# Optimization experiments

Measured on AMD Instinct MI355X. Metric: run time of the kernel, lower is better.

## Reference

```python
import jax, jax.numpy as jnp
import numpy as np

# ---- model dims ----
D_MODEL = 256; D_STATE = 128; D_CONV = 4; EXPAND = 2; HEADDIM = 64
D_INNER = EXPAND * D_MODEL            # 512
NHEADS = D_INNER // HEADDIM           # 8
CONV_DIM = D_INNER + 2 * D_STATE      # 768
D_IN_PROJ = 2 * D_INNER + 2 * D_STATE + NHEADS  # 1288
N_GENES = 4095; BATCH = 4; CHUNK = 64
GENE_ID_DIM = 64; PATH_DIM = 128; CHR_DIM = 16; N_CHROM = 25; LFF = 32
GENE_FEAT_DIM = GENE_ID_DIM + PATH_DIM + 2 * CHR_DIM  # 224
N_PERT = 2048; PERT_DIM = 128


def silu(x):
    return x * jax.nn.sigmoid(x)


def segsum_exp(a):
    # a: (..., T). Returns lower-triangular exp(sum_{k=j+1..i} a_k), zero above diag.
    T = a.shape[-1]
    cs = jnp.cumsum(a, axis=-1)
    d = cs[..., :, None] - cs[..., None, :]
    mask = jnp.tril(jnp.ones((T, T), dtype=bool))
    return jnp.exp(jnp.where(mask, d, 0.0)) * mask


def ssd(X, A, B, C):
    # Chunked SSD (Mamba2 selective scan). X:(b,l,h,p) pre-multiplied by dt,
    # A:(b,l,h) = a*dt, B/C:(b,l,n) (ngroups=1 broadcast over heads).
    b, l, h, p = X.shape
    n = B.shape[-1]
    c = l // CHUNK
    Xc = X.reshape(b, c, CHUNK, h, p)
    Bc = B.reshape(b, c, CHUNK, n)
    Cc = C.reshape(b, c, CHUNK, n)
    Ac = A.reshape(b, c, CHUNK, h).transpose(0, 3, 1, 2)  # (b,h,c,cl)
    A_cs = jnp.cumsum(Ac, axis=-1)
    L = segsum_exp(Ac)                                     # (b,h,c,cl,cl)
    Y_diag = jnp.einsum('bcln,bcsn,bhcls,bcshp->bclhp', Cc, Bc, L, Xc)
    decay_states = jnp.exp(A_cs[..., -1:] - A_cs)          # (b,h,c,cl)
    states = jnp.einsum('bcln,bhcl,bclhp->bchpn', Bc, decay_states, Xc)
    chunk_decay = jnp.exp(A_cs[..., -1])                   # (b,h,c)

    def step(h_prev, inp):
        dec, s = inp
        return h_prev * dec[..., None, None] + s, h_prev

    init = jnp.zeros((b, h, p, n), X.dtype)
    _, prev = jax.lax.scan(step, init, (chunk_decay.transpose(2, 0, 1),
                                        states.transpose(1, 0, 2, 3, 4)))
    prev = prev.transpose(1, 0, 2, 3, 4)                   # (b,c,h,p,n)
    Y_off = jnp.einsum('bcln,bchpn,bhcl->bclhp', Cc, prev, jnp.exp(A_cs))
    return (Y_diag + Y_off).reshape(b, l, h, p)


def mamba2(x, in_w, conv_w, conv_b, dt_bias, A_log, D, norm_w, out_w):
    b, l, _ = x.shape
    zxbcdt = x @ in_w.T                                    # (b,l,1288)
    z = zxbcdt[..., :D_INNER]
    xBC = zxbcdt[..., D_INNER:D_INNER + CONV_DIM]
    dt = jax.nn.softplus(zxbcdt[..., D_INNER + CONV_DIM:] + dt_bias)  # (b,l,h)
    # causal depthwise conv1d
    xc = jax.lax.conv_general_dilated(
        xBC.transpose(0, 2, 1), conv_w[:, None, :], (1,), [(D_CONV - 1, 0)],
        feature_group_count=CONV_DIM,
        dimension_numbers=('NCH', 'OIH', 'NCH'))
    xBC = silu(xc.transpose(0, 2, 1) + conv_b)
    xs = xBC[..., :D_INNER].reshape(b, l, NHEADS, HEADDIM)
    Bm = xBC[..., D_INNER:D_INNER + D_STATE]
    Cm = xBC[..., D_INNER + D_STATE:]
    A = -jnp.exp(A_log)                                    # (h,)
    y = ssd(xs * dt[..., None], dt * A, Bm, Cm) + D[:, None] * xs
    y = y.reshape(b, l, D_INNER)
    y = y * silu(z)                                        # gated RMSNorm
    y = y * jax.lax.rsqrt(jnp.mean(y * y, axis=-1, keepdims=True) + 1e-5) * norm_w
    return y @ out_w.T


def _forward(perturbation_idx, chr_idx, locus_fourier, pathway_features,
             gene_id_emb, chr_emb, locus_w, locus_b, pert_emb, cond_w, cond_b,
             inp_w, inp_b, ln_g, ln_b,
             mf_in_w, mf_conv_w, mf_conv_b, mf_dt_bias, mf_A_log, mf_D, mf_norm_w, mf_out_w,
             mb_in_w, mb_conv_w, mb_conv_b, mb_dt_bias, mb_A_log, mb_D, mb_norm_w, mb_out_w,
             head_w, head_b):
    e_locus = jax.nn.gelu(locus_fourier @ locus_w.T + locus_b, approximate=False)
    gene_feat = jnp.concatenate(
        [gene_id_emb, pathway_features, chr_emb[chr_idx], e_locus], axis=-1)  # (G,224)
    cond = pert_emb[perturbation_idx] @ cond_w.T + cond_b                      # (B,224)
    seq = jnp.concatenate(
        [cond[:, None, :],
         jnp.broadcast_to(gene_feat[None], (BATCH, N_GENES, GENE_FEAT_DIM))], axis=1)
    seq = seq @ inp_w.T + inp_b                                                # (B,4096,256)
    mu = jnp.mean(seq, axis=-1, keepdims=True)
    var = jnp.var(seq, axis=-1, keepdims=True)
    seq = (seq - mu) * jax.lax.rsqrt(var + 1e-5) * ln_g + ln_b
    # L = 4096 is already a multiple of 16 -> no padding branch.
    h_fwd = mamba2(seq, mf_in_w, mf_conv_w, mf_conv_b, mf_dt_bias, mf_A_log, mf_D, mf_norm_w, mf_out_w)
    h_bwd = jnp.flip(mamba2(jnp.flip(seq, 1), mb_in_w, mb_conv_w, mb_conv_b, mb_dt_bias, mb_A_log, mb_D, mb_norm_w, mb_out_w), 1)
    H = h_fwd + h_bwd
    return H[:, 1:, :] @ head_w.T + head_b                                     # (B,4095,1)


def setup_inputs() -> dict:
    key = jax.random.key(0)
    ks = iter(jax.random.split(key, 64))

    def nrm(shape, s=0.02):
        return jax.random.normal(next(ks), shape, jnp.float32) * s

    inp = {}
    inp['perturbation_idx'] = jax.random.randint(next(ks), (BATCH,), 0, N_PERT)
    inp['chr_idx'] = jax.random.randint(next(ks), (N_GENES,), 0, N_CHROM)
    inp['locus_fourier'] = nrm((N_GENES, 2 * LFF), 1.0)
    inp['pathway_features'] = nrm((N_GENES, PATH_DIM), 1.0)
    inp['gene_id_emb'] = nrm((N_GENES, GENE_ID_DIM))
    inp['chr_emb'] = nrm((N_CHROM, CHR_DIM))
    inp['locus_w'] = nrm((CHR_DIM, 2 * LFF)); inp['locus_b'] = jnp.zeros((CHR_DIM,))
    inp['pert_emb'] = nrm((N_PERT, PERT_DIM))
    inp['cond_w'] = nrm((GENE_FEAT_DIM, PERT_DIM)); inp['cond_b'] = jnp.zeros((GENE_FEAT_DIM,))
    inp['inp_w'] = nrm((D_MODEL, GENE_FEAT_DIM)); inp['inp_b'] = jnp.zeros((D_MODEL,))
    inp['ln_g'] = jnp.ones((D_MODEL,)); inp['ln_b'] = jnp.zeros((D_MODEL,))
    for pre in ('mf_', 'mb_'):
        inp[pre + 'in_w'] = nrm((D_IN_PROJ, D_MODEL))
        inp[pre + 'conv_w'] = nrm((CONV_DIM, D_CONV), 0.2)
        inp[pre + 'conv_b'] = jnp.zeros((CONV_DIM,))
        inp[pre + 'dt_bias'] = nrm((NHEADS,), 0.5)
        inp[pre + 'A_log'] = jnp.log(jax.random.uniform(next(ks), (NHEADS,), jnp.float32, 1.0, 16.0))
        inp[pre + 'D'] = jnp.ones((NHEADS,))
        inp[pre + 'norm_w'] = jnp.ones((D_INNER,))
        inp[pre + 'out_w'] = nrm((D_MODEL, D_INNER))
    inp['head_w'] = nrm((1, D_MODEL)); inp['head_b'] = jnp.zeros((1,))
    return inp


def reference(perturbation_idx, chr_idx, locus_fourier, pathway_features,
              gene_id_emb, chr_emb, locus_w, locus_b, pert_emb, cond_w, cond_b,
              inp_w, inp_b, ln_g, ln_b,
              mf_in_w, mf_conv_w, mf_conv_b, mf_dt_bias, mf_A_log, mf_D, mf_norm_w, mf_out_w,
              mb_in_w, mb_conv_w, mb_conv_b, mb_dt_bias, mb_A_log, mb_D, mb_norm_w, mb_out_w,
              head_w, head_b):
    return _forward(perturbation_idx, chr_idx, locus_fourier, pathway_features,
                    gene_id_emb, chr_emb, locus_w, locus_b, pert_emb, cond_w, cond_b,
                    inp_w, inp_b, ln_g, ln_b,
                    mf_in_w, mf_conv_w, mf_conv_b, mf_dt_bias, mf_A_log, mf_D, mf_norm_w, mf_out_w,
                    mb_in_w, mb_conv_w, mb_conv_b, mb_dt_bias, mb_A_log, mb_D, mb_norm_w, mb_out_w,
                    head_w, head_b)
```

## Files before the change

### kernel.cpp

```cpp
#include <hip/hip_runtime.h>
#include <hip/hip_bf16.h>
#include <math.h>

#define LSEQ   4096
#define NGENES 4095
#define NB     4
#define DM     256
#define DI     512
#define DST    128
#define NH     8
#define HD     64
#define CONVD  768
#define DIP    1288
#define NCHK   64
#define CHK    64
#define GFD    224

#define ZN  ((size_t)NB*LSEQ*DI)
#define XN  ((size_t)NB*LSEQ*CONVD)
#define DN  ((size_t)NB*LSEQ*NH)
#define AN  ((size_t)NB*NH*LSEQ)
#define SN  ((size_t)NB*NCHK*NH*HD*DST)
#define GN  ((size_t)NB*NCHK*CHK*CHK)
#define BTN ((size_t)NB*NCHK*DST*CHK)
#define HN  ((size_t)NB*LSEQ*DM)

typedef short bf16x8 __attribute__((ext_vector_type(8)));
typedef short bf16x4 __attribute__((ext_vector_type(4)));
typedef float f32x4 __attribute__((ext_vector_type(4)));

__device__ __forceinline__ float bf2f(unsigned short u){
    unsigned int x = ((unsigned int)u) << 16;
    return __uint_as_float(x);
}
__device__ __forceinline__ unsigned short f2bf(float f){
    __hip_bfloat16 h = __float2bfloat16(f);
    return *reinterpret_cast<unsigned short*>(&h);
}

typedef const __attribute__((address_space(1))) void* gas_t;
typedef __attribute__((address_space(3))) void* las_t;
__device__ __forceinline__ void gload16(const void* g, void* l){
    __builtin_amdgcn_global_load_lds((gas_t)g, (las_t)l, 16, 0, 0);
}

__global__ void k_detect(const unsigned int* p, int* flag){
    *flag = (*p == 0x3F803F80u) ? 1 : 0;
}

struct ConvAll { const void* src[31]; float* dst[31]; int n[31]; };
__global__ void k_convert_all(ConvAll a, const int* flag){
    int ai = blockIdx.y;
    int n = a.n[ai];
    const void* s = a.src[ai]; float* d = a.dst[ai];
    bool bf = (*flag != 0);
    for(int i = blockIdx.x*256 + threadIdx.x; i < n; i += gridDim.x*256){
        d[i] = bf ? bf2f(((const unsigned short*)s)[i]) : ((const float*)s)[i];
    }
}

struct PackAll { const void* src[4]; unsigned short* dst[4]; int n[4]; };
__global__ void k_pack_all(PackAll a, const int* flag){
    int ai = blockIdx.y;
    int n = a.n[ai];
    const void* s = a.src[ai]; unsigned short* d = a.dst[ai];
    bool bf = (*flag != 0);
    for(int i = blockIdx.x*256 + threadIdx.x; i < n; i += gridDim.x*256){
        if(bf) d[i] = ((const unsigned short*)s)[i];
        else   d[i] = f2bf(((const float*)s)[i]);
    }
}

__global__ void k_packw256(const void* src, unsigned short* dst, const int* flag){
    int row = blockIdx.x, col = threadIdx.x;
    unsigned short v = 0;
    if(col < GFD){
        if(*flag) v = ((const unsigned short*)src)[row*GFD + col];
        else      v = f2bf(((const float*)src)[row*GFD + col]);
    }
    dst[row*256 + col] = v;
}

__global__ void k_genefeat(const float* gene_id, const float* pathway, const float* chr_emb,
                           const int* chr_idx, const float* lf, const float* locus_w,
                           const float* locus_b, unsigned short* gfb){
    int g = blockIdx.x; int t = threadIdx.x;
    float v = 0.f;
    if(t < 64)       v = gene_id[g*64 + t];
    else if(t < 192) v = pathway[g*128 + (t-64)];
    else if(t < 208) v = chr_emb[chr_idx[g]*16 + (t-192)];
    else if(t < 224){
        int j = t - 208;
        float acc = locus_b[j];
        for(int k=0;k<64;k++) acc += lf[g*64+k]*locus_w[j*64+k];
        v = 0.5f*acc*(1.0f + erff(acc*0.7071067811865475f));
    }
    gfb[g*256 + t] = f2bf(v);
}

__global__ void k_cond(const int* pidx, const float* pert_emb, const float* cond_w,
                       const float* cond_b, unsigned short* condb){
    int b = blockIdx.x, t = threadIdx.x;
    float acc = 0.f;
    if(t < GFD){
        const float* pe = pert_emb + pidx[b]*128;
        acc = cond_b[t];
        for(int k=0;k<128;k++) acc += pe[k]*cond_w[t*128+k];
    }
    condb[b*256 + t] = f2bf(acc);
}

__global__ __launch_bounds__(256) void k_mm_seqpre(const unsigned short* gfb,
            const unsigned short* condb, const unsigned short* Wb,
            const float* inp_b, float* seq_pre){
    __shared__ unsigned short sh[16384];
    int sblk = (blockIdx.x & 7)*32 + (blockIdx.x >> 3);
    int bm = sblk>>1, bn = sblk&1;
    int m0 = bm*128, n0 = bn*128;
    int t = threadIdx.x, lane = t&63;
    int wid = t>>6, wm = wid>>1, wn = wid&1;
    int fr = lane&15, fk = lane>>4;
    int srow = t>>3;
    int scol = ((t&7) ^ (srow&7))*8;
    const unsigned short* gA[4]; const unsigned short* gB[4];
#pragma unroll
    for(int q=0;q<4;q++){
        int row = q*32 + srow;
        int m = m0+row; int b = m>>12, l = m&4095;
        gA[q] = l ? &gfb[(size_t)(l-1)*256 + scol] : &condb[(size_t)b*256 + scol];
        gB[q] = &Wb[(size_t)(n0+row)*256 + scol];
    }
    unsigned short* lA = &sh[t*8];
    unsigned short* lB = &sh[8192 + t*8];
    f32x4 acc[4][4];
#pragma unroll
    for(int i=0;i<4;i++)
#pragma unroll
        for(int j=0;j<4;j++) acc[i][j] = (f32x4){0.f,0.f,0.f,0.f};
    for(int it=0; it<4; it++){
#pragma unroll
        for(int q=0;q<4;q++){
            gload16(gA[q], lA + q*2048);
            gload16(gB[q], lB + q*2048);
            gA[q] += 64; gB[q] += 64;
        }
        __syncthreads();
#pragma unroll
        for(int kk8=0;kk8<8;kk8+=4){
            bf16x8 av[4], bv[4];
#pragma unroll
            for(int i=0;i<4;i++){
                int r = wm*64+i*16+fr;
                av[i] = *(bf16x8*)&sh[r*64 + (((kk8+fk)^(r&7))*8)];
            }
#pragma unroll
            for(int j=0;j<4;j++){
                int r = wn*64+j*16+fr;
                bv[j] = *(bf16x8*)&sh[8192 + r*64 + (((kk8+fk)^(r&7))*8)];
            }
#pragma unroll
            for(int i=0;i<4;i++)
#pragma unroll
                for(int j=0;j<4;j++)
                    acc[i][j] = __builtin_amdgcn_mfma_f32_16x16x32_bf16(av[i], bv[j], acc[i][j], 0,0,0);
        }
        __syncthreads();
    }
#pragma unroll
    for(int i=0;i<4;i++)
#pragma unroll
        for(int rr=0;rr<4;rr++){
            int m = m0 + wm*64 + i*16 + fk*4 + rr;
#pragma unroll
            for(int j=0;j<4;j++){
                int n = n0 + wn*64 + j*16 + fr;
                seq_pre[(size_t)m*256 + n] = acc[i][j][rr] + inp_b[n];
            }
        }
}

__global__ void k_ln(const float* seq_pre, const float* ln_g, const float* ln_b,
                     unsigned short* seqb){
    int t = threadIdx.x; int w = t>>6, lane = t&63;
    int m = blockIdx.x*4 + w;
    f32x4 v = *(const f32x4*)&seq_pre[(size_t)m*256 + lane*4];
    float s1 = v[0]+v[1]+v[2]+v[3];
    float s2 = v[0]*v[0]+v[1]*v[1]+v[2]*v[2]+v[3]*v[3];
#pragma unroll
    for(int o=32;o>0;o>>=1){ s1 += __shfl_xor(s1,o,64); s2 += __shfl_xor(s2,o,64); }
    float mu  = s1*(1.f/256.f);
    float var = s2*(1.f/256.f) - mu*mu;
    float rs = rsqrtf(var+1e-5f);
    unsigned short o4[4];
#pragma unroll
    for(int j=0;j<4;j++){
        int n = lane*4+j;
        o4[j] = f2bf((v[j]-mu)*rs*ln_g[n] + ln_b[n]);
    }
    *(unsigned long long*)&seqb[(size_t)m*256 + lane*4] = *(unsigned long long*)o4;
}

__global__ __launch_bounds__(256) void k_mm_inproj(const unsigned short* seqb,
            const unsigned short* W0, const unsigned short* W1,
            const float* dtb0, const float* dtb1,
            unsigned short* zbase, unsigned short* xbase, float* dtbase){
    __shared__ unsigned short sh[16384];
    int blk = (blockIdx.x & 7)*352 + (blockIdx.x >> 3);
    int dir = blk >= 1408; int inner = blk - dir*1408;
    int bm = inner/11, bn = inner%11;
    int m0 = bm*128, n0 = bn*128;
    const unsigned short* Wb = dir ? W1 : W0;
    const float* dt_bias = dir ? dtb1 : dtb0;
    unsigned short* zb   = zbase + (size_t)dir*ZN;
    unsigned short* xbcr = xbase + (size_t)dir*XN;
    float* dtb = dtbase + (size_t)dir*DN;
    int t = threadIdx.x, lane = t&63;
    int wid = t>>6, wm = wid>>1, wn = wid&1;
    int fr = lane&15, fk = lane>>4;
    int srow = t>>3;
    int scol = ((t&7) ^ (srow&7))*8;
    const unsigned short* gA[4]; const unsigned short* gB[4];
#pragma unroll
    for(int q=0;q<4;q++){
        int row = q*32 + srow;
        int m = m0+row; int b = m>>12, l = m&4095;
        int ml = dir ? (4095-l) : l;
        gA[q] = &seqb[(size_t)(b*4096+ml)*256 + scol];
        gB[q] = &Wb[(size_t)(n0+row)*256 + scol];
    }
    unsigned short* lA = &sh[t*8];
    unsigned short* lB = &sh[8192 + t*8];
    f32x4 acc[4][4];
#pragma unroll
    for(int i=0;i<4;i++)
#pragma unroll
        for(int j=0;j<4;j++) acc[i][j] = (f32x4){0.f,0.f,0.f,0.f};
    for(int it=0; it<4; it++){
#pragma unroll
        for(int q=0;q<4;q++){
            gload16(gA[q], lA + q*2048);
            gload16(gB[q], lB + q*2048);
            gA[q] += 64; gB[q] += 64;
        }
        __syncthreads();
#pragma unroll
        for(int kk8=0;kk8<8;kk8+=4){
            bf16x8 av[4], bv[4];
#pragma unroll
            for(int i=0;i<4;i++){
                int r = wm*64+i*16+fr;
                av[i] = *(bf16x8*)&sh[r*64 + (((kk8+fk)^(r&7))*8)];
            }
#pragma unroll
            for(int j=0;j<4;j++){
                int r = wn*64+j*16+fr;
                bv[j] = *(bf16x8*)&sh[8192 + r*64 + (((kk8+fk)^(r&7))*8)];
            }
#pragma unroll
            for(int i=0;i<4;i++)
#pragma unroll
                for(int j=0;j<4;j++)
                    acc[i][j] = __builtin_amdgcn_mfma_f32_16x16x32_bf16(av[i], bv[j], acc[i][j], 0,0,0);
        }
        __syncthreads();
    }
    if(bn == 10){
#pragma unroll
        for(int i=0;i<4;i++)
#pragma unroll
            for(int rr=0;rr<4;rr++){
                int m = m0 + wm*64 + i*16 + fk*4 + rr;
#pragma unroll
                for(int j=0;j<4;j++){
                    int n = n0 + wn*64 + j*16 + fr;
                    if(n >= DIP) continue;
                    int hh = n - 1280;
                    float x = acc[i][j][rr] + dt_bias[hh];
                    dtb[(size_t)m*NH + hh] = (x > 20.f) ? x : log1pf(expf(x));
                }
            }
        return;
    }
    unsigned short* dst; int stride, coff;
    if(bn < 4){ dst = zb;   stride = DI;    coff = bn*128; }
    else      { dst = xbcr; stride = CONVD; coff = bn*128 - 512; }
#pragma unroll
    for(int p=0;p<2;p++){
        if(wm == p){
#pragma unroll
            for(int i=0;i<4;i++)
#pragma unroll
                for(int j=0;j<4;j++)
#pragma unroll
                    for(int rr=0;rr<4;rr++){
                        int row = i*16 + fk*4 + rr;
                        int col = wn*64 + j*16 + fr;
                        sh[row*136 + col] = f2bf(acc[i][j][rr]);
                    }
        }
        __syncthreads();
#pragma unroll
        for(int k=0;k<4;k++){
            int idx = t + k*256;
            int row = idx>>4, c8 = (idx&15)*8;
            bf16x8 v = *(bf16x8*)&sh[row*136 + c8];
            *(bf16x8*)&dst[(size_t)(m0+p*64+row)*stride + coff + c8] = v;
        }
        __syncthreads();
    }
}

__global__ __launch_bounds__(256) void k_conv(const unsigned short* xbase,
        const float* cw0, const float* cw1, const float* cb0, const float* cb1,
        unsigned short* obase){
    __shared__ unsigned short raw[19*768];
    __shared__ float cwf[4*768];
    __shared__ float cbf[768];
    int blk = blockIdx.x;
    int dir = blk>>10; int rem = blk&1023;
    int b = rem>>8, rg = rem&255;
    const unsigned short* xr = xbase + (size_t)dir*XN;
    unsigned short* out = obase + (size_t)dir*XN;
    const float* cw = dir ? cw1 : cw0;
    const float* cb = dir ? cb1 : cb0;
    int l0 = rg*16;
    int t = threadIdx.x;
    for(int i=t;i<3072;i+=256){ int q=i/768, c=i%768; cwf[q*768+c] = cw[c*4+q]; }
    for(int i=t;i<768;i+=256) cbf[i] = cb[i];
    for(int i=t;i<19*96;i+=256){
        int r = i/96, c8 = (i%96)*8;
        int l = l0 - 3 + r;
        bf16x8 v = (bf16x8){0,0,0,0,0,0,0,0};
        if(l >= 0) v = *(const bf16x8*)&xr[(size_t)(b*4096+l)*768 + c8];
        *(bf16x8*)&raw[r*768 + c8] = v;
    }
    __syncthreads();
    for(int i=t;i<16*96;i+=256){
        int r = i/96, c8 = (i%96)*8;
        bf16x8 o;
#pragma unroll
        for(int j=0;j<8;j++){
            int c = c8+j;
            float acc = cbf[c];
#pragma unroll
            for(int q=0;q<4;q++) acc += cwf[q*768+c]*bf2f(raw[(r+q)*768 + c]);
            o[j] = (short)f2bf(acc/(1.f+__expf(-acc)));
        }
        *(bf16x8*)&out[(size_t)(b*4096+l0+r)*768 + c8] = o;
    }
}

__global__ void k_cumsum(const float* dtbase, const float* Al0, const float* Al1,
                         float* acsbase){
    __shared__ float tmp[64];
    int blk = blockIdx.x;
    int dir = blk>>11; int rem = blk&2047;
    int c = rem & 63; int bh = rem >> 6; int h = bh & 7; int b = bh >> 3;
    const float* dtb = dtbase + (size_t)dir*DN;
    float* acs = acsbase + (size_t)dir*AN;
    int s = threadIdx.x;
    float A = -expf((dir?Al1:Al0)[h]);
    int l = c*64 + s;
    tmp[s] = dtb[(size_t)(b*4096+l)*NH + h] * A;
    __syncthreads();
    if(s == 0){ for(int i=1;i<64;i++) tmp[i] += tmp[i-1]; }
    __syncthreads();
    acs[(size_t)(b*8+h)*4096 + l] = tmp[s];
}

__global__ __launch_bounds__(256) void k_cbprep(const unsigned short* xbase,
        unsigned short* Gbase, unsigned short* BTbase){
    __shared__ unsigned short Bb[64][136];
    __shared__ unsigned short Cb[64][136];
    __shared__ unsigned short BTs[128][72];
    int blk = blockIdx.x;
    int dir = blk>>8; int bc = blk&255;
    int b = bc>>6, c = bc&63;
    const unsigned short* xbcb = xbase + (size_t)dir*XN;
    unsigned short* Gb = Gbase + (size_t)dir*GN;
    unsigned short* BTg = BTbase + (size_t)dir*BTN;
    int t = threadIdx.x, lane = t&63, wid = t>>6;
    int fr = lane&15, fk = lane>>4;
    size_t rowbase = (size_t)(b*4096 + c*64)*CONVD;
#pragma unroll
    for(int q=0;q<4;q++){
        int e = t + q*256; int r = e>>4, ch = (e&15)*8;
        *(bf16x8*)&Bb[r][ch] = *(const bf16x8*)&xbcb[rowbase + (size_t)r*CONVD + 512 + ch];
        *(bf16x8*)&Cb[r][ch] = *(const bf16x8*)&xbcb[rowbase + (size_t)r*CONVD + 640 + ch];
    }
    __syncthreads();
    f32x4 g[4];
#pragma unroll
    for(int j=0;j<4;j++) g[j] = (f32x4){0.f,0.f,0.f,0.f};
#pragma unroll
    for(int k0=0;k0<128;k0+=32){
        bf16x8 av = *(bf16x8*)&Cb[wid*16+fr][k0+fk*8];
#pragma unroll
        for(int j=0;j<4;j++){
            bf16x8 bv = *(bf16x8*)&Bb[j*16+fr][k0+fk*8];
            g[j] = __builtin_amdgcn_mfma_f32_16x16x32_bf16(av, bv, g[j], 0,0,0);
        }
    }
    size_t gbase = (size_t)bc*4096;
#pragma unroll
    for(int j=0;j<4;j++)
#pragma unroll
        for(int rr=0;rr<4;rr++)
            Gb[gbase + (size_t)(wid*16+fk*4+rr)*64 + j*16+fr] = f2bf(g[j][rr]);
#pragma unroll
    for(int q=0;q<4;q++){
        int e = t + q*256; int s = e>>4, n0 = (e&15)*8;
        bf16x8 v = *(bf16x8*)&Bb[s][n0];
#pragma unroll
        for(int j=0;j<8;j++){
            int n = n0 + j;
            BTs[n][s ^ (n&56)] = (unsigned short)v[j];
        }
    }
    __syncthreads();
    size_t btbase = (size_t)bc*8192;
#pragma unroll
    for(int q=0;q<4;q++){
        int e = t + q*256; int n = e>>3, s0 = (e&7)*8;
        bf16x8 v = *(bf16x8*)&BTs[n][s0 ^ (n&56)];
        *(bf16x8*)&BTg[btbase + (size_t)n*64 + s0] = v;
    }
}

#define G_OFF  0
#define BT_OFF 4608
#define XT_OFF 13824
#define MS_OFF 18432
__global__ __launch_bounds__(256) void k_ssd_intra(const unsigned short* xbase,
        const unsigned short* Gbase, const unsigned short* BTbase,
        const float* dtbase, const float* acsbase,
        const float* Dv0, const float* Dv1,
        unsigned short* Ybase, unsigned short* sbase_){
    __shared__ unsigned short sh[23040];
    __shared__ float acs_s[64], dts[64], ws[64];
    int blk = blockIdx.x;
    int dir = blk>>9; int rem = blk&511;
    int hg = rem&1, c = (rem>>1)&63, b = rem>>7;
    int bc = b*64 + c;
    const unsigned short* xbcb = xbase + (size_t)dir*XN;
    const unsigned short* Gb = Gbase + (size_t)dir*GN;
    const unsigned short* BTg = BTbase + (size_t)dir*BTN;
    const float* dtb = dtbase + (size_t)dir*DN;
    const float* acs = acsbase + (size_t)dir*AN;
    const float* Dv = dir ? Dv1 : Dv0;
    unsigned short* Yb = Ybase + (size_t)dir*XN;
    unsigned short* states = sbase_ + (size_t)dir*SN;
    int t = threadIdx.x, lane = t&63, wid = t>>6;
    int wr = wid>>1, wc = wid&1;
    int fr = lane&15, fk = lane>>4;
    size_t rowbase = (size_t)(b*4096 + c*64)*CONVD;
    size_t gbase = (size_t)bc*4096;
    size_t btbase = (size_t)bc*8192;
#pragma unroll
    for(int q=0;q<2;q++){
        int e = t + q*256; int l = e>>3, s0 = (e&7)*8;
        *(bf16x8*)&sh[G_OFF + l*72 + s0] = *(const bf16x8*)&Gb[gbase + (size_t)l*64 + s0];
    }
#pragma unroll
    for(int q=0;q<4;q++){
        int e = t + q*256; int n = e>>3, s0 = (e&7)*8;
        *(bf16x8*)&sh[BT_OFF + n*72 + (s0 ^ (n&56))] = *(const bf16x8*)&BTg[btbase + (size_t)n*64 + s0];
    }
    for(int hh=0; hh<4; hh++){
        int h = hg*4 + hh;
        __syncthreads();
#pragma unroll
        for(int q=0;q<2;q++){
            int e = t + q*256; int s = e>>3, p0 = (e&7)*8;
            bf16x8 v = *(const bf16x8*)&xbcb[rowbase + (size_t)s*CONVD + h*64 + p0];
            int sw = s ^ (p0&56);
#pragma unroll
            for(int j=0;j<8;j++) sh[XT_OFF + (p0+j)*72 + sw] = (unsigned short)v[j];
        }
        if(t < 64){
            acs_s[t] = acs[(size_t)(b*8+h)*4096 + c*64 + t];
            dts[t]   = dtb[(size_t)(b*4096 + c*64 + t)*NH + h];
        }
        __syncthreads();
        if(t < 64) ws[t] = __expf(acs_s[63]-acs_s[t])*dts[t];
#pragma unroll
        for(int q=0;q<16;q++){
            int e = t + q*256; int l = e>>6, s = e&63;
            float m = (s <= l) ? bf2f(sh[G_OFF + l*72 + s])*__expf(acs_s[l]-acs_s[s])*dts[s] : 0.f;
            sh[MS_OFF + l*72 + s] = f2bf(m);
        }
        __syncthreads();
        f32x4 y[2][2];
#pragma unroll
        for(int i=0;i<2;i++)
#pragma unroll
            for(int j=0;j<2;j++) y[i][j] = (f32x4){0.f,0.f,0.f,0.f};
#pragma unroll
        for(int k0=0;k0<64;k0+=32){
            bf16x8 av[2], bv[2];
#pragma unroll
            for(int i=0;i<2;i++) av[i] = *(bf16x8*)&sh[MS_OFF + (wr*32+i*16+fr)*72 + k0+fk*8];
#pragma unroll
            for(int j=0;j<2;j++){
                int p = wc*32+j*16+fr;
                bv[j] = *(bf16x8*)&sh[XT_OFF + p*72 + ((k0+fk*8) ^ (p&56))];
            }
#pragma unroll
            for(int i=0;i<2;i++)
#pragma unroll
                for(int j=0;j<2;j++)
                    y[i][j] = __builtin_amdgcn_mfma_f32_16x16x32_bf16(av[i], bv[j], y[i][j], 0,0,0);
        }
        __syncthreads();
        float Dh = Dv[h];
#pragma unroll
        for(int i=0;i<2;i++)
#pragma unroll
            for(int j=0;j<2;j++)
#pragma unroll
                for(int rr=0;rr<4;rr++){
                    int l = wr*32 + i*16 + fk*4 + rr;
                    int p = wc*32 + j*16 + fr;
                    float xv = bf2f(sh[XT_OFF + p*72 + (l ^ (p&56))]);
                    sh[MS_OFF + l*72 + p] = f2bf(y[i][j][rr] + Dh*xv);
                }
        f32x4 s4[2][4];
#pragma unroll
        for(int i=0;i<2;i++)
#pragma unroll
            for(int j=0;j<4;j++) s4[i][j] = (f32x4){0.f,0.f,0.f,0.f};
#pragma unroll
        for(int k0=0;k0<64;k0+=32){
            bf16x8 av[2], bv[4];
#pragma unroll
            for(int i=0;i<2;i++){
                int p = wr*32+i*16+fr;
                bf16x8 raw = *(bf16x8*)&sh[XT_OFF + p*72 + ((k0+fk*8) ^ (p&56))];
#pragma unroll
                for(int e=0;e<8;e++) av[i][e] = (short)f2bf(bf2f((unsigned short)raw[e]) * ws[k0+fk*8+e]);
            }
#pragma unroll
            for(int j=0;j<4;j++){
                int n = wc*64+j*16+fr;
                bv[j] = *(bf16x8*)&sh[BT_OFF + n*72 + ((k0+fk*8) ^ (n&56))];
            }
#pragma unroll
            for(int i=0;i<2;i++)
#pragma unroll
                for(int j=0;j<4;j++)
                    s4[i][j] = __builtin_amdgcn_mfma_f32_16x16x32_bf16(av[i], bv[j], s4[i][j], 0,0,0);
        }
        __syncthreads();
#pragma unroll
        for(int k=0;k<2;k++){
            int e = t + k*256; int row = e>>3, c8 = (e&7)*8;
            bf16x8 v = *(bf16x8*)&sh[MS_OFF + row*72 + c8];
            *(bf16x8*)&Yb[(size_t)(b*4096 + c*64 + row)*DI + h*64 + c8] = v;
        }
        __syncthreads();
#pragma unroll
        for(int i=0;i<2;i++)
#pragma unroll
            for(int j=0;j<4;j++)
#pragma unroll
                for(int rr=0;rr<4;rr++){
                    int p = wr*32 + i*16 + fk*4 + rr;
                    int n = wc*64 + j*16 + fr;
                    sh[XT_OFF + p*128 + (n ^ ((p&7)<<3))] = f2bf(s4[i][j][rr]);
                }
        __syncthreads();
        size_t sb = ((size_t)bc*8 + h)*8192;
#pragma unroll
        for(int k=0;k<4;k++){
            int e = t + k*256; int p = e>>4, c8 = (e&15)*8;
            bf16x8 v = *(bf16x8*)&sh[XT_OFF + p*128 + (c8 ^ ((p&7)<<3))];
            *(bf16x8*)&states[sb + p*128 + c8] = v;
        }
    }
}

__global__ void k_scan(unsigned short* sbase_, const float* acsbase){
    __shared__ float dec_s[64];
    int blk = blockIdx.x;
    int dir = blk>>8; int rem = blk&255;
    int e8 = rem&7, h = (rem>>3)&7, b = rem>>6;
    unsigned short* states = sbase_ + (size_t)dir*SN;
    const float* acs = acsbase + (size_t)dir*AN;
    int t = threadIdx.x;
    if(t < 64) dec_s[t] = __expf(acs[(size_t)(b*8+h)*4096 + t*64 + 63]);
    __syncthreads();
    int off = e8*1024 + t*4;
    float h4[4] = {0.f,0.f,0.f,0.f};
    size_t base0 = ((size_t)(b*64)*8 + h)*8192 + off;
    for(int c0=0;c0<64;c0+=4){
        bf16x4 v[4];
#pragma unroll
        for(int u=0;u<4;u++)
            v[u] = *(const bf16x4*)&states[base0 + (size_t)(c0+u)*65536];
#pragma unroll
        for(int u=0;u<4;u++){
            float dec = dec_s[c0+u];
            bf16x4 o;
#pragma unroll
            for(int j=0;j<4;j++){
                o[j] = (short)f2bf(h4[j]);
                h4[j] = h4[j]*dec + bf2f((unsigned short)v[u][j]);
            }
            *(bf16x4*)&states[base0 + (size_t)(c0+u)*65536] = o;
        }
    }
}

__global__ __launch_bounds__(256) void k_ssd_off(unsigned short* xbase,
        const unsigned short* sbase_, const float* acsbase){
    __shared__ unsigned short Ct[64][136];
    __shared__ unsigned short Pv[64][136];
    __shared__ float acs_s[64];
    int blk = blockIdx.x;
    int dir = blk>>8; int bc = blk&255;
    int c = bc&63, b = bc>>6;
    unsigned short* xbcb = xbase + (size_t)dir*XN;
    const unsigned short* prev = sbase_ + (size_t)dir*SN;
    const float* acs = acsbase + (size_t)dir*AN;
    int t = threadIdx.x, lane = t&63, wid = t>>6;
    int wr = wid>>1, wc = wid&1;
    int fr = lane&15, fk = lane>>4;
    size_t rowbase = (size_t)(b*4096 + c*64)*CONVD;
    unsigned short* ostg = &Pv[0][0];
#pragma unroll
    for(int q=0;q<4;q++){
        int e = t + q*256;
        int r = e>>4, ch = (e&15)*8;
        *(bf16x8*)&Ct[r][ch] = *(const bf16x8*)&xbcb[rowbase + (size_t)r*CONVD + 640 + ch];
    }
    for(int h=0; h<8; h++){
        size_t sb = ((size_t)bc*8 + h)*8192;
        __syncthreads();
#pragma unroll
        for(int q=0;q<4;q++){
            int e = t + q*256;
            int r = e>>4, ch = (e&15)*8;
            *(bf16x8*)&Pv[r][ch] = *(const bf16x8*)&prev[sb + (size_t)r*128 + ch];
        }
        if(t < 64) acs_s[t] = acs[(size_t)(b*8+h)*4096 + c*64 + t];
        __syncthreads();
        f32x4 o[2][2];
#pragma unroll
        for(int i=0;i<2;i++)
#pragma unroll
            for(int j=0;j<2;j++) o[i][j] = (f32x4){0.f,0.f,0.f,0.f};
        for(int k0=0;k0<128;k0+=32){
            bf16x8 av[2], bv[2];
#pragma unroll
            for(int i=0;i<2;i++) av[i] = *(bf16x8*)&Ct[wr*32+i*16+fr][k0+fk*8];
#pragma unroll
            for(int j=0;j<2;j++) bv[j] = *(bf16x8*)&Pv[wc*32+j*16+fr][k0+fk*8];
#pragma unroll
            for(int i=0;i<2;i++)
#pragma unroll
                for(int j=0;j<2;j++)
                    o[i][j] = __builtin_amdgcn_mfma_f32_16x16x32_bf16(av[i], bv[j], o[i][j], 0,0,0);
        }
        __syncthreads();
#pragma unroll
        for(int i=0;i<2;i++)
#pragma unroll
            for(int j=0;j<2;j++)
#pragma unroll
                for(int rr=0;rr<4;rr++){
                    int l = wr*32 + i*16 + fk*4 + rr;
                    int p = wc*32 + j*16 + fr;
                    ostg[l*72 + p] = f2bf(o[i][j][rr]*__expf(acs_s[l]));
                }
        __syncthreads();
#pragma unroll
        for(int k=0;k<2;k++){
            int e = t + k*256; int row = e>>3, c8 = (e&7)*8;
            bf16x8 v = *(bf16x8*)&ostg[row*72 + c8];
            *(bf16x8*)&xbcb[rowbase + (size_t)row*CONVD + h*64 + c8] = v;
        }
    }
}

__global__ void k_gate(const unsigned short* Ybase, const unsigned short* xbase,
                       const unsigned short* zbase,
                       const float* nw0, const float* nw1, unsigned short* ynbase){
    int blk = blockIdx.x;
    int dir = blk>>12;
    int t = threadIdx.x; int w = t>>6, lane = t&63;
    int m = (blk&4095)*4 + w;
    const unsigned short* Yb = Ybase + (size_t)dir*XN;
    const unsigned short* Ob = xbase + (size_t)dir*XN;
    const unsigned short* zb = zbase + (size_t)dir*ZN;
    unsigned short* ynb = ynbase + (size_t)dir*SN;
    const float* norm_w = dir ? nw1 : nw0;
    size_t base = (size_t)m*DI + lane*8;
    bf16x8 yv = *(const bf16x8*)&Yb[base];
    bf16x8 ov = *(const bf16x8*)&Ob[(size_t)m*CONVD + lane*8];
    bf16x8 zv = *(const bf16x8*)&zb[base];
    float v[8]; float ss = 0.f;
#pragma unroll
    for(int j=0;j<8;j++){
        float zf = bf2f((unsigned short)zv[j]);
        float yt = bf2f((unsigned short)yv[j]) + bf2f((unsigned short)ov[j]);
        float f = yt * (zf/(1.f+__expf(-zf)));
        v[j] = f; ss += f*f;
    }
#pragma unroll
    for(int o=32;o>0;o>>=1) ss += __shfl_xor(ss,o,64);
    float r = rsqrtf(ss*(1.f/512.f) + 1e-5f);
    bf16x8 o8;
#pragma unroll
    for(int j=0;j<8;j++) o8[j] = (short)f2bf(v[j]*r*norm_w[lane*8+j]);
    *(bf16x8*)&ynb[base] = o8;
}

__global__ __launch_bounds__(256) void k_mm_outproj(const unsigned short* ynbase,
            const unsigned short* W0, const unsigned short* W1, float* Hbase){
    __shared__ unsigned short sh[16384];
    int blk = (blockIdx.x & 7)*64 + (blockIdx.x >> 3);
    int dir = blk>>8; int rem = blk&255;
    int bm = rem>>1, bn = rem&1;
    int m0 = bm*128, n0 = bn*128;
    const unsigned short* ynb = ynbase + (size_t)dir*SN;
    const unsigned short* Wb = dir ? W1 : W0;
    float* H = Hbase + (size_t)dir*HN;
    int t = threadIdx.x, lane = t&63;
    int wid = t>>6, wm = wid>>1, wn = wid&1;
    int fr = lane&15, fk = lane>>4;
    int srow = t>>3;
    int scol = ((t&7) ^ (srow&7))*8;
    const unsigned short* gA[4]; const unsigned short* gB[4];
#pragma unroll
    for(int q=0;q<4;q++){
        int row = q*32 + srow;
        gA[q] = &ynb[(size_t)(m0+row)*512 + scol];
        gB[q] = &Wb[(size_t)(n0+row)*512 + scol];
    }
    unsigned short* lA = &sh[t*8];
    unsigned short* lB = &sh[8192 + t*8];
    f32x4 acc[4][4];
#pragma unroll
    for(int i=0;i<4;i++)
#pragma unroll
        for(int j=0;j<4;j++) acc[i][j] = (f32x4){0.f,0.f,0.f,0.f};
    for(int it=0; it<8; it++){
#pragma unroll
        for(int q=0;q<4;q++){
            gload16(gA[q], lA + q*2048);
            gload16(gB[q], lB + q*2048);
            gA[q] += 64; gB[q] += 64;
        }
        __syncthreads();
#pragma unroll
        for(int kk8=0;kk8<8;kk8+=4){
            bf16x8 av[4], bv[4];
#pragma unroll
            for(int i=0;i<4;i++){
                int r = wm*64+i*16+fr;
                av[i] = *(bf16x8*)&sh[r*64 + (((kk8+fk)^(r&7))*8)];
            }
#pragma unroll
            for(int j=0;j<4;j++){
                int r = wn*64+j*16+fr;
                bv[j] = *(bf16x8*)&sh[8192 + r*64 + (((kk8+fk)^(r&7))*8)];
            }
#pragma unroll
            for(int i=0;i<4;i++)
#pragma unroll
                for(int j=0;j<4;j++)
                    acc[i][j] = __builtin_amdgcn_mfma_f32_16x16x32_bf16(av[i], bv[j], acc[i][j], 0,0,0);
        }
        __syncthreads();
    }
#pragma unroll
    for(int i=0;i<4;i++)
#pragma unroll
        for(int rr=0;rr<4;rr++){
            int m = m0 + wm*64 + i*16 + fk*4 + rr;
            int b = m>>12, l = m&4095;
            int ml = dir ? (4095 - l) : l;
#pragma unroll
            for(int j=0;j<4;j++){
                int n = n0 + wn*64 + j*16 + fr;
                H[(size_t)(b*4096+ml)*256 + n] = acc[i][j][rr];
            }
        }
}

__global__ void k_head(const float* H0, const float* H1, const float* head_w,
                       const float* head_b, void* out, const int* flag){
    int t = threadIdx.x; int w = t>>6, lane = t&63;
    int row = blockIdx.x*4 + w;
    int b = row/4095, g = row - b*4095;
    size_t idx = ((size_t)(b*4096) + g + 1)*256 + lane*4;
    f32x4 h0 = *(const f32x4*)&H0[idx];
    f32x4 h1 = *(const f32x4*)&H1[idx];
    f32x4 wv = *(const f32x4*)&head_w[lane*4];
    float ss = (h0[0]+h1[0])*wv[0]+(h0[1]+h1[1])*wv[1]+(h0[2]+h1[2])*wv[2]+(h0[3]+h1[3])*wv[3];
#pragma unroll
    for(int o=32;o>0;o>>=1) ss += __shfl_xor(ss,o,64);
    if(lane == 0){
        float val = ss + head_b[0];
        if(*flag) ((__hip_bfloat16*)out)[b*4095 + g] = __float2bfloat16(val);
        else      ((float*)out)[b*4095 + g] = val;
    }
}

extern "C" void kernel_launch(void* const* d_in, const int* in_sizes, int n_in,
                              void* d_out, int out_size, void* d_ws, size_t ws_size,
                              hipStream_t stream){
    if(n_in < 33){
        hipMemsetAsync(d_out, 0, (size_t)out_size*2, stream);
        return;
    }
    char* base = (char*)d_ws;
    size_t off = 256;
    int* flag = (int*)base;
    auto alloc = [&](size_t nbytes)->char*{
        char* p = base + off;
        off += ((nbytes + 255) & ~(size_t)255);
        return p;
    };
    float* F[33];
    for(int i=0;i<33;i++){
        if(i==0 || i==1 || i==11 || i==15 || i==22 || i==23 || i==30){ F[i] = nullptr; continue; }
        F[i] = (float*)alloc((size_t)in_sizes[i]*4);
    }
    unsigned short* inwb[2];
    unsigned short* outwb[2];
    inwb[0]  = (unsigned short*)alloc((size_t)DIP*DM*2);
    inwb[1]  = (unsigned short*)alloc((size_t)DIP*DM*2);
    outwb[0] = (unsigned short*)alloc((size_t)DM*DI*2);
    outwb[1] = (unsigned short*)alloc((size_t)DM*DI*2);
    unsigned short* inpwb = (unsigned short*)alloc((size_t)DM*256*2);
    unsigned short* gfb   = (unsigned short*)alloc((size_t)NGENES*256*2);
    unsigned short* condb = (unsigned short*)alloc((size_t)NB*256*2);
    unsigned short* seqb  = (unsigned short*)alloc((size_t)NB*LSEQ*DM*2);
    float* H0      = (float*)alloc(HN*4);
    float* H1      = (float*)alloc(HN*4);
    unsigned short* zb   = (unsigned short*)alloc(ZN*2*2);
    unsigned short* xbcr = (unsigned short*)alloc(XN*2*2);
    unsigned short* xbcb = (unsigned short*)alloc(XN*2*2);
    float* dtb     = (float*)alloc(DN*2*4);
    float* acs     = (float*)alloc(AN*2*4);
    unsigned short* states = (unsigned short*)alloc(SN*2*2);
    unsigned short* Gb  = (unsigned short*)H0;
    unsigned short* BTg = (unsigned short*)((char*)H0 + ((GN*2*2 + 255) & ~(size_t)255));
    float* seq_pre = (float*)xbcr;
    unsigned short* Ybuf = xbcr;
    unsigned short* ynb = states;
    if(off > ws_size){
        hipMemsetAsync(d_out, 0, (size_t)out_size*2, stream);
        return;
    }

    k_detect<<<1,1,0,stream>>>((const unsigned int*)d_in[13], flag);

    ConvAll ca;
    for(int i=2;i<33;i++){
        int ai = i-2;
        ca.src[ai] = d_in[i];
        ca.dst[ai] = F[i];
        int n = in_sizes[i];
        if(i==11 || i==15 || i==22 || i==23 || i==30) n = 0;
        ca.n[ai] = n;
    }
    k_convert_all<<<dim3(96,31),256,0,stream>>>(ca, flag);

    PackAll pa;
    pa.src[0] = d_in[15]; pa.dst[0] = inwb[0];  pa.n[0] = DIP*DM;
    pa.src[1] = d_in[23]; pa.dst[1] = inwb[1];  pa.n[1] = DIP*DM;
    pa.src[2] = d_in[22]; pa.dst[2] = outwb[0]; pa.n[2] = DM*DI;
    pa.src[3] = d_in[30]; pa.dst[3] = outwb[1]; pa.n[3] = DM*DI;
    k_pack_all<<<dim3(64,4),256,0,stream>>>(pa, flag);
    k_packw256<<<DM,256,0,stream>>>(d_in[11], inpwb, flag);

    k_genefeat<<<NGENES,256,0,stream>>>(F[4], F[3], F[5], (const int*)d_in[1],
                                        F[2], F[6], F[7], gfb);
    k_cond<<<NB,256,0,stream>>>((const int*)d_in[0], F[8], F[9], F[10], condb);
    k_mm_seqpre<<<128*2,256,0,stream>>>(gfb, condb, inpwb, F[12], seq_pre);
    k_ln<<<NB*LSEQ/4,256,0,stream>>>(seq_pre, F[13], F[14], seqb);

    k_mm_inproj<<<2816,256,0,stream>>>(seqb, inwb[0], inwb[1], F[18], F[26],
                                       zb, xbcr, dtb);
    k_conv<<<2048,256,0,stream>>>(xbcr, F[16], F[24], F[17], F[25], xbcb);
    k_cumsum<<<4096,64,0,stream>>>(dtb, F[19], F[27], acs);
    k_cbprep<<<512,256,0,stream>>>(xbcb, Gb, BTg);
    k_ssd_intra<<<1024,256,0,stream>>>(xbcb, Gb, BTg, dtb, acs, F[20], F[28],
                                       Ybuf, states);
    k_scan<<<512,256,0,stream>>>(states, acs);
    k_ssd_off<<<512,256,0,stream>>>(xbcb, states, acs);
    k_gate<<<8192,256,0,stream>>>(Ybuf, xbcb, zb, F[21], F[29], ynb);
    k_mm_outproj<<<512,256,0,stream>>>(ynb, outwb[0], outwb[1], H0);

    k_head<<<NB*NGENES/4,256,0,stream>>>(H0, H1, F[31], F[32], d_out, flag);
}
```

Baseline: 280.4 us.

## Read raw inputs directly, shrink conversions, bf16 outproj output, shuffle cumsum

Gene-feature and condition kernels now read the raw inputs directly with a bf16/fp32 flag, so those large tables are no longer converted up front. The convert kernel gets a much smaller grid. The cumsum uses a wavefront shuffle scan instead of a serial loop in shared memory, and the SSD intra kernel reads G from global memory instead of staging it in LDS. The scan kernel prefetches the next group of states, and the output projection writes bf16 through an LDS transpose so the head kernel reads half the bytes. The bf16 output adds rounding error before the head reduction.

```diff
diff --git a/kernel.cpp b/kernel.cpp
--- a/kernel.cpp
+++ b/kernel.cpp
@@ -37,6 +37,9 @@
     __hip_bfloat16 h = __float2bfloat16(f);
     return *reinterpret_cast<unsigned short*>(&h);
 }
+__device__ __forceinline__ float ldraw(const void* p, size_t i, bool bf){
+    return bf ? bf2f(((const unsigned short*)p)[i]) : ((const float*)p)[i];
+}
 
 typedef const __attribute__((address_space(1))) void* gas_t;
 typedef __attribute__((address_space(3))) void* las_t;
@@ -81,31 +84,33 @@
     dst[row*256 + col] = v;
 }
 
-__global__ void k_genefeat(const float* gene_id, const float* pathway, const float* chr_emb,
-                           const int* chr_idx, const float* lf, const float* locus_w,
-                           const float* locus_b, unsigned short* gfb){
+__global__ void k_genefeat(const void* gene_id, const void* pathway, const void* chr_emb,
+                           const int* chr_idx, const void* lf, const void* locus_w,
+                           const void* locus_b, unsigned short* gfb, const int* flag){
     int g = blockIdx.x; int t = threadIdx.x;
+    bool bf = (*flag != 0);
     float v = 0.f;
-    if(t < 64)       v = gene_id[g*64 + t];
-    else if(t < 192) v = pathway[g*128 + (t-64)];
-    else if(t < 208) v = chr_emb[chr_idx[g]*16 + (t-192)];
+    if(t < 64)       v = ldraw(gene_id, (size_t)g*64 + t, bf);
+    else if(t < 192) v = ldraw(pathway, (size_t)g*128 + (t-64), bf);
+    else if(t < 208) v = ldraw(chr_emb, (size_t)chr_idx[g]*16 + (t-192), bf);
     else if(t < 224){
         int j = t - 208;
-        float acc = locus_b[j];
-        for(int k=0;k<64;k++) acc += lf[g*64+k]*locus_w[j*64+k];
+        float acc = ldraw(locus_b, j, bf);
+        for(int k=0;k<64;k++) acc += ldraw(lf,(size_t)g*64+k,bf)*ldraw(locus_w,(size_t)j*64+k,bf);
         v = 0.5f*acc*(1.0f + erff(acc*0.7071067811865475f));
     }
     gfb[g*256 + t] = f2bf(v);
 }
 
-__global__ void k_cond(const int* pidx, const float* pert_emb, const float* cond_w,
-                       const float* cond_b, unsigned short* condb){
+__global__ void k_cond(const int* pidx, const void* pert_emb, const void* cond_w,
+                       const void* cond_b, unsigned short* condb, const int* flag){
     int b = blockIdx.x, t = threadIdx.x;
+    bool bf = (*flag != 0);
     float acc = 0.f;
     if(t < GFD){
-        const float* pe = pert_emb + pidx[b]*128;
-        acc = cond_b[t];
-        for(int k=0;k<128;k++) acc += pe[k]*cond_w[t*128+k];
+        size_t pe = (size_t)pidx[b]*128;
+        acc = ldraw(cond_b, t, bf);
+        for(int k=0;k<128;k++) acc += ldraw(pert_emb, pe+k, bf)*ldraw(cond_w,(size_t)t*128+k,bf);
     }
     condb[b*256 + t] = f2bf(acc);
 }
@@ -352,7 +357,6 @@
 
 __global__ void k_cumsum(const float* dtbase, const float* Al0, const float* Al1,
                          float* acsbase){
-    __shared__ float tmp[64];
     int blk = blockIdx.x;
     int dir = blk>>11; int rem = blk&2047;
     int c = rem & 63; int bh = rem >> 6; int h = bh & 7; int b = bh >> 3;
@@ -361,11 +365,13 @@
     int s = threadIdx.x;
     float A = -expf((dir?Al1:Al0)[h]);
     int l = c*64 + s;
-    tmp[s] = dtb[(size_t)(b*4096+l)*NH + h] * A;
-    __syncthreads();
-    if(s == 0){ for(int i=1;i<64;i++) tmp[i] += tmp[i-1]; }
-    __syncthreads();
-    acs[(size_t)(b*8+h)*4096 + l] = tmp[s];
+    float v = dtb[(size_t)(b*4096+l)*NH + h] * A;
+#pragma unroll
+    for(int o=1;o<64;o<<=1){
+        float u = __shfl_up(v, o, 64);
+        if(s >= o) v += u;
+    }
+    acs[(size_t)(b*8+h)*4096 + l] = v;
 }
 
 __global__ __launch_bounds__(256) void k_cbprep(const unsigned short* xbase,
@@ -427,16 +433,15 @@
     }
 }
 
-#define G_OFF  0
-#define BT_OFF 4608
-#define XT_OFF 13824
-#define MS_OFF 18432
+#define BT_OFF 0
+#define XT_OFF 9216
+#define MS_OFF 13824
 __global__ __launch_bounds__(256) void k_ssd_intra(const unsigned short* xbase,
         const unsigned short* Gbase, const unsigned short* BTbase,
         const float* dtbase, const float* acsbase,
         const float* Dv0, const float* Dv1,
         unsigned short* Ybase, unsigned short* sbase_){
-    __shared__ unsigned short sh[23040];
+    __shared__ unsigned short sh[18432];
     __shared__ float acs_s[64], dts[64], ws[64];
     int blk = blockIdx.x;
     int dir = blk>>9; int rem = blk&511;
@@ -457,11 +462,6 @@
     size_t gbase = (size_t)bc*4096;
     size_t btbase = (size_t)bc*8192;
 #pragma unroll
-    for(int q=0;q<2;q++){
-        int e = t + q*256; int l = e>>3, s0 = (e&7)*8;
-        *(bf16x8*)&sh[G_OFF + l*72 + s0] = *(const bf16x8*)&Gb[gbase + (size_t)l*64 + s0];
-    }
-#pragma unroll
     for(int q=0;q<4;q++){
         int e = t + q*256; int n = e>>3, s0 = (e&7)*8;
         *(bf16x8*)&sh[BT_OFF + n*72 + (s0 ^ (n&56))] = *(const bf16x8*)&BTg[btbase + (size_t)n*64 + s0];
@@ -486,7 +486,7 @@
 #pragma unroll
         for(int q=0;q<16;q++){
             int e = t + q*256; int l = e>>6, s = e&63;
-            float m = (s <= l) ? bf2f(sh[G_OFF + l*72 + s])*__expf(acs_s[l]-acs_s[s])*dts[s] : 0.f;
+            float m = (s <= l) ? bf2f(Gb[gbase + (size_t)l*64 + s])*__expf(acs_s[l]-acs_s[s])*dts[s] : 0.f;
             sh[MS_OFF + l*72 + s] = f2bf(m);
         }
         __syncthreads();
@@ -592,11 +592,14 @@
     int off = e8*1024 + t*4;
     float h4[4] = {0.f,0.f,0.f,0.f};
     size_t base0 = ((size_t)(b*64)*8 + h)*8192 + off;
+    bf16x4 v[4], vn[4];
+#pragma unroll
+    for(int u=0;u<4;u++) v[u] = *(const bf16x4*)&states[base0 + (size_t)u*65536];
     for(int c0=0;c0<64;c0+=4){
-        bf16x4 v[4];
-#pragma unroll
-        for(int u=0;u<4;u++)
-            v[u] = *(const bf16x4*)&states[base0 + (size_t)(c0+u)*65536];
+        if(c0+4 < 64){
+#pragma unroll
+            for(int u=0;u<4;u++) vn[u] = *(const bf16x4*)&states[base0 + (size_t)(c0+4+u)*65536];
+        }
 #pragma unroll
         for(int u=0;u<4;u++){
             float dec = dec_s[c0+u];
@@ -608,6 +611,8 @@
             }
             *(bf16x4*)&states[base0 + (size_t)(c0+u)*65536] = o;
         }
+#pragma unroll
+        for(int u=0;u<4;u++) v[u] = vn[u];
     }
 }
 
@@ -716,7 +721,7 @@
 }
 
 __global__ __launch_bounds__(256) void k_mm_outproj(const unsigned short* ynbase,
-            const unsigned short* W0, const unsigned short* W1, float* Hbase){
+            const unsigned short* W0, const unsigned short* W1, unsigned short* Hbase){
     __shared__ unsigned short sh[16384];
     int blk = (blockIdx.x & 7)*64 + (blockIdx.x >> 3);
     int dir = blk>>8; int rem = blk&255;
@@ -724,7 +729,7 @@
     int m0 = bm*128, n0 = bn*128;
     const unsigned short* ynb = ynbase + (size_t)dir*SN;
     const unsigned short* Wb = dir ? W1 : W0;
-    float* H = Hbase + (size_t)dir*HN;
+    unsigned short* H = Hbase + (size_t)dir*HN;
     int t = threadIdx.x, lane = t&63;
     int wid = t>>6, wm = wid>>1, wn = wid&1;
     int fr = lane&15, fk = lane>>4;
@@ -774,30 +779,47 @@
         __syncthreads();
     }
 #pragma unroll
-    for(int i=0;i<4;i++)
-#pragma unroll
-        for(int rr=0;rr<4;rr++){
-            int m = m0 + wm*64 + i*16 + fk*4 + rr;
+    for(int p=0;p<2;p++){
+        if(wm == p){
+#pragma unroll
+            for(int i=0;i<4;i++)
+#pragma unroll
+                for(int j=0;j<4;j++)
+#pragma unroll
+                    for(int rr=0;rr<4;rr++){
+                        int row = i*16 + fk*4 + rr;
+                        int col = wn*64 + j*16 + fr;
+                        sh[row*136 + col] = f2bf(acc[i][j][rr]);
+                    }
+        }
+        __syncthreads();
+#pragma unroll
+        for(int k=0;k<4;k++){
+            int idx = t + k*256;
+            int row = idx>>4, c8 = (idx&15)*8;
+            int m = m0 + p*64 + row;
             int b = m>>12, l = m&4095;
             int ml = dir ? (4095 - l) : l;
-#pragma unroll
-            for(int j=0;j<4;j++){
-                int n = n0 + wn*64 + j*16 + fr;
-                H[(size_t)(b*4096+ml)*256 + n] = acc[i][j][rr];
-            }
-        }
-}
-
-__global__ void k_head(const float* H0, const float* H1, const float* head_w,
+            bf16x8 v = *(bf16x8*)&sh[row*136 + c8];
+            *(bf16x8*)&H[(size_t)(b*4096+ml)*256 + n0 + c8] = v;
+        }
+        __syncthreads();
+    }
+}
+
+__global__ void k_head(const unsigned short* Hb, const float* head_w,
                        const float* head_b, void* out, const int* flag){
     int t = threadIdx.x; int w = t>>6, lane = t&63;
     int row = blockIdx.x*4 + w;
     int b = row/4095, g = row - b*4095;
     size_t idx = ((size_t)(b*4096) + g + 1)*256 + lane*4;
-    f32x4 h0 = *(const f32x4*)&H0[idx];
-    f32x4 h1 = *(const f32x4*)&H1[idx];
+    bf16x4 h0 = *(const bf16x4*)&Hb[idx];
+    bf16x4 h1 = *(const bf16x4*)&Hb[HN + idx];
     f32x4 wv = *(const f32x4*)&head_w[lane*4];
-    float ss = (h0[0]+h1[0])*wv[0]+(h0[1]+h1[1])*wv[1]+(h0[2]+h1[2])*wv[2]+(h0[3]+h1[3])*wv[3];
+    float ss = 0.f;
+#pragma unroll
+    for(int j=0;j<4;j++)
+        ss += (bf2f((unsigned short)h0[j]) + bf2f((unsigned short)h1[j]))*wv[j];
 #pragma unroll
     for(int o=32;o>0;o>>=1) ss += __shfl_xor(ss,o,64);
     if(lane == 0){
@@ -823,9 +845,13 @@
         return p;
     };
     float* F[33];
-    for(int i=0;i<33;i++){
-        if(i==0 || i==1 || i==11 || i==15 || i==22 || i==23 || i==30){ F[i] = nullptr; continue; }
-        F[i] = (float*)alloc((size_t)in_sizes[i]*4);
+    for(int i=0;i<33;i++) F[i] = nullptr;
+    {
+        const int need[] = {12,13,14,16,17,18,19,20,21,24,25,26,27,28,29,31,32};
+        for(int k=0;k<(int)(sizeof(need)/sizeof(int));k++){
+            int i = need[k];
+            F[i] = (float*)alloc((size_t)in_sizes[i]*4);
+        }
     }
     unsigned short* inwb[2];
     unsigned short* outwb[2];
@@ -837,16 +863,15 @@
     unsigned short* gfb   = (unsigned short*)alloc((size_t)NGENES*256*2);
     unsigned short* condb = (unsigned short*)alloc((size_t)NB*256*2);
     unsigned short* seqb  = (unsigned short*)alloc((size_t)NB*LSEQ*DM*2);
-    float* H0      = (float*)alloc(HN*4);
-    float* H1      = (float*)alloc(HN*4);
+    unsigned short* Hb    = (unsigned short*)alloc(HN*2*2);
     unsigned short* zb   = (unsigned short*)alloc(ZN*2*2);
     unsigned short* xbcr = (unsigned short*)alloc(XN*2*2);
     unsigned short* xbcb = (unsigned short*)alloc(XN*2*2);
     float* dtb     = (float*)alloc(DN*2*4);
     float* acs     = (float*)alloc(AN*2*4);
     unsigned short* states = (unsigned short*)alloc(SN*2*2);
-    unsigned short* Gb  = (unsigned short*)H0;
-    unsigned short* BTg = (unsigned short*)((char*)H0 + ((GN*2*2 + 255) & ~(size_t)255));
+    unsigned short* Gb  = Hb;
+    unsigned short* BTg = (unsigned short*)((char*)Hb + ((GN*2*2 + 255) & ~(size_t)255));
     float* seq_pre = (float*)xbcr;
     unsigned short* Ybuf = xbcr;
     unsigned short* ynb = states;
@@ -862,11 +887,9 @@
         int ai = i-2;
         ca.src[ai] = d_in[i];
         ca.dst[ai] = F[i];
-        int n = in_sizes[i];
-        if(i==11 || i==15 || i==22 || i==23 || i==30) n = 0;
-        ca.n[ai] = n;
-    }
-    k_convert_all<<<dim3(96,31),256,0,stream>>>(ca, flag);
+        ca.n[ai] = F[i] ? in_sizes[i] : 0;
+    }
+    k_convert_all<<<dim3(4,31),256,0,stream>>>(ca, flag);
 
     PackAll pa;
     pa.src[0] = d_in[15]; pa.dst[0] = inwb[0];  pa.n[0] = DIP*DM;
@@ -876,9 +899,9 @@
     k_pack_all<<<dim3(64,4),256,0,stream>>>(pa, flag);
     k_packw256<<<DM,256,0,stream>>>(d_in[11], inpwb, flag);
 
-    k_genefeat<<<NGENES,256,0,stream>>>(F[4], F[3], F[5], (const int*)d_in[1],
-                                        F[2], F[6], F[7], gfb);
-    k_cond<<<NB,256,0,stream>>>((const int*)d_in[0], F[8], F[9], F[10], condb);
+    k_genefeat<<<NGENES,256,0,stream>>>(d_in[4], d_in[3], d_in[5], (const int*)d_in[1],
+                                        d_in[2], d_in[6], d_in[7], gfb, flag);
+    k_cond<<<NB,256,0,stream>>>((const int*)d_in[0], d_in[8], d_in[9], d_in[10], condb, flag);
     k_mm_seqpre<<<128*2,256,0,stream>>>(gfb, condb, inpwb, F[12], seq_pre);
     k_ln<<<NB*LSEQ/4,256,0,stream>>>(seq_pre, F[13], F[14], seqb);
 
@@ -892,7 +915,7 @@
     k_scan<<<512,256,0,stream>>>(states, acs);
     k_ssd_off<<<512,256,0,stream>>>(xbcb, states, acs);
     k_gate<<<8192,256,0,stream>>>(Ybuf, xbcb, zb, F[21], F[29], ynb);
-    k_mm_outproj<<<512,256,0,stream>>>(ynb, outwb[0], outwb[1], H0);
-
-    k_head<<<NB*NGENES/4,256,0,stream>>>(H0, H1, F[31], F[32], d_out, flag);
-}
+    k_mm_outproj<<<512,256,0,stream>>>(ynb, outwb[0], outwb[1], Hb);
+
+    k_head<<<NB*NGENES/4,256,0,stream>>>(Hb, F[31], F[32], d_out, flag);
+}
```

New measurement: 299.2 us. 6.7% more time.
